# Kernel optimization log

Hardware: AMD Instinct MI355X
Metric: run time of the kernel (lower is better)

Reference implementation:

```python
import jax, jax.numpy as jnp
import numpy as np

N = 100000      # nodes
E = 1600000     # edges (avg degree 16)
IN = 256        # in_channels
HID = 128       # hidden_channels
K = 10          # APPNP propagation steps
ALPHA = 0.1     # APPNP teleport probability


def setup_inputs() -> dict:
    key = jax.random.key(0)
    k1, k2, k3 = jax.random.split(key, 3)
    features = jax.random.normal(k1, (N, IN), dtype=jnp.float32)
    W = jax.random.normal(k2, (IN, HID), dtype=jnp.float32) * (1.0 / np.sqrt(IN))
    b = jnp.zeros((HID,), dtype=jnp.float32)
    edge_index = jax.random.randint(k3, (2, E), 0, N, dtype=jnp.int32)
    return {"features": features, "W": W, "b": b, "edge_index": edge_index}


def _edge_norm(src, dst, n):
    # DGL GraphConv norm='both': D_out^{-1/2} at src, D_in^{-1/2} at dst
    ones = jnp.ones(src.shape, dtype=jnp.float32)
    deg_out = jax.ops.segment_sum(ones, src, num_segments=n)
    deg_in = jax.ops.segment_sum(ones, dst, num_segments=n)
    inv_out = jnp.where(deg_out > 0, jax.lax.rsqrt(jnp.maximum(deg_out, 1.0)), 0.0)
    inv_in = jnp.where(deg_in > 0, jax.lax.rsqrt(jnp.maximum(deg_in, 1.0)), 0.0)
    return inv_out[src] * inv_in[dst]  # [E] per-edge coefficient


def _propagate(h, src, dst, enorm, n):
    # gather src features, scale by symmetric norm, scatter-add to dst
    m = h[src] * enorm[:, None]                       # [E, HID]
    return jax.ops.segment_sum(m, dst, num_segments=n)


def reference(features, W, b, edge_index):
    n = features.shape[0]
    src, dst = edge_index[0], edge_index[1]
    enorm = _edge_norm(src, dst, n)

    # GraphConv: project then aggregate (feat dropout is identity in eval)
    h = features @ W                                  # [N, HID]
    h = _propagate(h, src, dst, enorm, n) + b
    h = jax.nn.relu(h)

    # APPNP: h_{t+1} = (1-alpha) * A_hat h_t + alpha * h_0 (edge_drop off in eval)
    h0 = h

    def step(hc, _):
        hn = (1.0 - ALPHA) * _propagate(hc, src, dst, enorm, n) + ALPHA * h0
        return hn, None

    h, _ = jax.lax.scan(step, h, None, length=K)
    return h
```

## Files before the change

kernel.cpp:

```cpp
#include <hip/hip_runtime.h>
#include <hip/hip_fp16.h>
#include <stdint.h>

#define N_NODES 100000
#define N_EDGES 1600000
#define IN_CH 256
#define HID 128
#define K_STEPS 10
#define ALPHA 0.1f

#define BKT_BITS 9
#define BKT_SIZE 512
#define NBKT 196
#define HBLK 256
#define EPB (N_EDGES / HBLK)

#define DR 8
#define DRS (N_NODES / DR)
#define DC 32
#define DCE (N_EDGES / DC)

static __global__ __launch_bounds__(256) void bucket_hist_kernel(const int* __restrict__ dst,
                                                                 uint32_t* __restrict__ partials) {
    __shared__ uint32_t h[NBKT];
    int b = blockIdx.x, t = threadIdx.x;
    if (t < NBKT) h[t] = 0;
    __syncthreads();
    int base = b * EPB;
    for (int i = t; i < EPB; i += 256)
        atomicAdd(&h[(unsigned)dst[base + i] >> BKT_BITS], 1u);
    __syncthreads();
    if (t < NBKT) partials[t * HBLK + b] = h[t];
}

static __global__ __launch_bounds__(256) void srcdeg_hist_kernel(const int* __restrict__ src,
                                                                 uint16_t* __restrict__ srcpart) {
    __shared__ uint32_t h[DRS];
    int r = blockIdx.x >> 5;
    int c = blockIdx.x & 31;
    int t = threadIdx.x;
    for (int i = t; i < DRS; i += 256) h[i] = 0;
    __syncthreads();
    int lo = r * DRS;
    int base = c * DCE;
    for (int i = t; i < DCE; i += 256) {
        unsigned sl = (unsigned)(src[base + i] - lo);
        if (sl < DRS) atomicAdd(&h[sl], 1u);
    }
    __syncthreads();
    for (int i = t; i < DRS; i += 256)
        srcpart[(size_t)c * N_NODES + lo + i] = (uint16_t)h[i];
}

static __global__ void srcdeg_reduce_kernel(const uint16_t* __restrict__ srcpart,
                                            float* __restrict__ inv_out) {
    int n = blockIdx.x * 256 + threadIdx.x;
    if (n >= N_NODES) return;
    uint32_t d = 0;
#pragma unroll
    for (int c = 0; c < DC; c++) d += srcpart[(size_t)c * N_NODES + n];
    inv_out[n] = d ? rsqrtf((float)d) : 0.f;
}

static __global__ __launch_bounds__(64) void bucket_totals_kernel(const uint32_t* __restrict__ partials,
                                                                  uint32_t* __restrict__ totals) {
    int k = blockIdx.x, t = threadIdx.x;
    const uint32_t* row = partials + (size_t)k * HBLK;
    uint32_t s = row[t] + row[t + 64] + row[t + 128] + row[t + 192];
#pragma unroll
    for (int o = 32; o; o >>= 1) s += __shfl_down(s, o);
    if (t == 0) totals[k] = s;
}

static __global__ __launch_bounds__(256) void bucket_cursor_kernel(const uint32_t* __restrict__ partials,
                                                                   const uint32_t* __restrict__ totals,
                                                                   uint32_t* __restrict__ blockCursor,
                                                                   uint32_t* __restrict__ bucket_base) {
    __shared__ uint32_t sc[256];
    int k = blockIdx.x, t = threadIdx.x;
    uint32_t tk = (t < NBKT) ? totals[t] : 0;
    sc[t] = tk;
    __syncthreads();
    for (int o = 1; o < 256; o <<= 1) {
        uint32_t u = (t >= o) ? sc[t - o] : 0;
        __syncthreads();
        sc[t] += u;
        __syncthreads();
    }
    uint32_t incl_k = sc[k];
    uint32_t total_k = totals[k];
    uint32_t base = incl_k - total_k;
    if (t == 0) {
        bucket_base[k] = base;
        if (k == NBKT - 1) bucket_base[NBKT] = incl_k;
    }
    __syncthreads();
    uint32_t p = partials[(size_t)k * HBLK + t];
    sc[t] = p;
    __syncthreads();
    for (int o = 1; o < 256; o <<= 1) {
        uint32_t u = (t >= o) ? sc[t - o] : 0;
        __syncthreads();
        sc[t] += u;
        __syncthreads();
    }
    blockCursor[(size_t)k * HBLK + t] = base + sc[t] - p;
}

static __global__ __launch_bounds__(256) void bucket_scatter_kernel(const int* __restrict__ src,
                                                                    const int* __restrict__ dst,
                                                                    const uint32_t* __restrict__ blockCursor,
                                                                    int2* __restrict__ ebuf) {
    __shared__ uint32_t cur[NBKT];
    int b = blockIdx.x, t = threadIdx.x;
    if (t < NBKT) cur[t] = blockCursor[(size_t)t * HBLK + b];
    __syncthreads();
    int base = b * EPB;
    for (int i = t; i < EPB; i += 256) {
        int s = src[base + i], d = dst[base + i];
        uint32_t p = atomicAdd(&cur[(unsigned)d >> BKT_BITS], 1u);
        ebuf[p] = make_int2(s, d);
    }
}

static __global__ __launch_bounds__(256) void bucket_build_kernel(const int2* __restrict__ ebuf,
                                                                  const uint32_t* __restrict__ bucket_base,
                                                                  int* __restrict__ row_ptr,
                                                                  float* __restrict__ inv_in,
                                                                  int* __restrict__ csr) {
    __shared__ uint32_t h[BKT_SIZE];
    __shared__ uint32_t rs[BKT_SIZE];
    __shared__ uint32_t ps[256];
    int k = blockIdx.x, t = threadIdx.x;
    uint32_t b0 = bucket_base[k], b1 = bucket_base[k + 1];
    h[t] = 0; h[t + 256] = 0;
    __syncthreads();
    for (uint32_t i = b0 + t; i < b1; i += 256)
        atomicAdd(&h[ebuf[i].y & (BKT_SIZE - 1)], 1u);
    __syncthreads();
    uint32_t a = h[2 * t], bb = h[2 * t + 1];
    uint32_t pair = a + bb;
    ps[t] = pair;
    __syncthreads();
    for (int o = 1; o < 256; o <<= 1) {
        uint32_t u = (t >= o) ? ps[t - o] : 0;
        __syncthreads();
        ps[t] += u;
        __syncthreads();
    }
    uint32_t ex = ps[t] - pair;
    rs[2 * t] = ex;
    rs[2 * t + 1] = ex + a;
    int node0 = k * BKT_SIZE;
    if (node0 + 2 * t < N_NODES) {
        row_ptr[node0 + 2 * t] = (int)(b0 + ex);
        inv_in[node0 + 2 * t] = a ? rsqrtf((float)a) : 0.f;
    }
    if (node0 + 2 * t + 1 < N_NODES) {
        row_ptr[node0 + 2 * t + 1] = (int)(b0 + ex + a);
        inv_in[node0 + 2 * t + 1] = bb ? rsqrtf((float)bb) : 0.f;
    }
    if (k == NBKT - 1 && t == 0) row_ptr[N_NODES] = (int)b1;
    __syncthreads();
    for (uint32_t i = b0 + t; i < b1; i += 256) {
        int2 e = ebuf[i];
        int li = e.y & (BKT_SIZE - 1);
        uint32_t p = atomicAdd(&rs[li], 1u);
        csr[b0 + p] = e.x;
    }
}

static __global__ __launch_bounds__(256) void gemm_kernel(const float* __restrict__ A,
                                                          const float* __restrict__ B,
                                                          const float* __restrict__ inv_out,
                                                          __half* __restrict__ t16) {
    __shared__ float As[32][68];
    __shared__ float Bs[32][128];
    int tid = threadIdx.x;
    int brow = blockIdx.x * 64;
    int tc = tid & 31, tr = tid >> 5;
    float acc[8][4] = {};
    for (int k0 = 0; k0 < IN_CH; k0 += 32) {
#pragma unroll
        for (int i = 0; i < 2; i++) {
            int l = (tid + i * 256) * 4;
            int r = l >> 5;
            int kk = l & 31;
            float4 a = make_float4(0.f, 0.f, 0.f, 0.f);
            int grow = brow + r;
            if (grow < N_NODES) a = *(const float4*)&A[(size_t)grow * IN_CH + k0 + kk];
            As[kk + 0][r] = a.x;
            As[kk + 1][r] = a.y;
            As[kk + 2][r] = a.z;
            As[kk + 3][r] = a.w;
        }
#pragma unroll
        for (int i = 0; i < 4; i++) {
            int l = (tid + i * 256) * 4;
            int kk = l >> 7;
            int cc = l & 127;
            *(float4*)&Bs[kk][cc] = *(const float4*)&B[(size_t)(k0 + kk) * HID + cc];
        }
        __syncthreads();
#pragma unroll
        for (int kk = 0; kk < 32; kk++) {
            float4 b4 = *(const float4*)&Bs[kk][tc * 4];
            float4 a0 = *(const float4*)&As[kk][tr * 8];
            float4 a1 = *(const float4*)&As[kk][tr * 8 + 4];
            float av[8] = {a0.x, a0.y, a0.z, a0.w, a1.x, a1.y, a1.z, a1.w};
#pragma unroll
            for (int i = 0; i < 8; i++) {
                acc[i][0] += av[i] * b4.x;
                acc[i][1] += av[i] * b4.y;
                acc[i][2] += av[i] * b4.z;
                acc[i][3] += av[i] * b4.w;
            }
        }
        __syncthreads();
    }
#pragma unroll
    for (int i = 0; i < 8; i++) {
        int grow = brow + tr * 8 + i;
        if (grow < N_NODES) {
            float sc = inv_out[grow];
            __half2 h01 = __floats2half2_rn(acc[i][0] * sc, acc[i][1] * sc);
            __half2 h23 = __floats2half2_rn(acc[i][2] * sc, acc[i][3] * sc);
            uint2 u;
            u.x = *(uint32_t*)&h01;
            u.y = *(uint32_t*)&h23;
            *(uint2*)&t16[(size_t)grow * HID + tc * 4] = u;
        }
    }
}

static __global__ void zero_rows_kernel(__half* a, __half* b, __half* c) {
    int t = threadIdx.x;
    ((uint32_t*)a)[(size_t)N_NODES * 64 + t] = 0;
    ((uint32_t*)b)[(size_t)N_NODES * 64 + t] = 0;
    ((uint32_t*)c)[(size_t)N_NODES * 64 + t] = 0;
}

template <int MODE>
static __global__ __launch_bounds__(256) void prop16_kernel(const __half* __restrict__ gin,
                                                            const int* __restrict__ rp,
                                                            const int* __restrict__ cs,
                                                            const float* __restrict__ inv_in,
                                                            const float* __restrict__ inv_out,
                                                            const float* __restrict__ bias,
                                                            const __half* __restrict__ h0h,
                                                            __half* __restrict__ gout,
                                                            __half* __restrict__ h0out,
                                                            float* __restrict__ fout) {
    int wid = (int)((blockIdx.x * 256u + threadIdx.x) >> 6);
    if (wid >= N_NODES) return;
    int lane = threadIdx.x & 63;
    int sub = lane >> 4;
    int cl = lane & 15;
    int s = rp[wid], e = rp[wid + 1];
    const uint4* g4 = (const uint4*)gin;

    float a[8] = {};
    for (int j = s; j < e; j += 8) {
        int j0 = j + sub, j1 = j0 + 4;
        int v0 = cs[j0], v1 = cs[j1];
        int i0 = (j0 < e) ? v0 : N_NODES;
        int i1 = (j1 < e) ? v1 : N_NODES;
        uint4 u0 = g4[(size_t)i0 * 16 + cl];
        uint4 u1 = g4[(size_t)i1 * 16 + cl];
        const __half2* p0 = (const __half2*)&u0;
        const __half2* p1 = (const __half2*)&u1;
#pragma unroll
        for (int k = 0; k < 4; k++) {
            float2 f0 = __half22float2(p0[k]);
            float2 f1 = __half22float2(p1[k]);
            a[2 * k] += f0.x + f1.x;
            a[2 * k + 1] += f0.y + f1.y;
        }
    }
#pragma unroll
    for (int k = 0; k < 8; k++) {
        a[k] += __shfl_xor(a[k], 16);
        a[k] += __shfl_xor(a[k], 32);
    }
    if (sub != 0) return;
    int c0 = cl * 8;
    if (MODE == 0) {
        float ii = inv_in[wid], io = inv_out[wid];
        float4 b0 = *(const float4*)&bias[c0];
        float4 b1 = *(const float4*)&bias[c0 + 4];
        float h[8];
        h[0] = fmaxf(a[0] * ii + b0.x, 0.f);
        h[1] = fmaxf(a[1] * ii + b0.y, 0.f);
        h[2] = fmaxf(a[2] * ii + b0.z, 0.f);
        h[3] = fmaxf(a[3] * ii + b0.w, 0.f);
        h[4] = fmaxf(a[4] * ii + b1.x, 0.f);
        h[5] = fmaxf(a[5] * ii + b1.y, 0.f);
        h[6] = fmaxf(a[6] * ii + b1.z, 0.f);
        h[7] = fmaxf(a[7] * ii + b1.w, 0.f);
        __half2 hh[4], gg[4];
#pragma unroll
        for (int k = 0; k < 4; k++) {
            hh[k] = __floats2half2_rn(h[2 * k], h[2 * k + 1]);
            gg[k] = __floats2half2_rn(h[2 * k] * io, h[2 * k + 1] * io);
        }
        ((uint4*)h0out)[(size_t)wid * 16 + cl] = *(uint4*)hh;
        ((uint4*)gout)[(size_t)wid * 16 + cl] = *(uint4*)gg;
    } else {
        float ii = inv_in[wid] * (1.f - ALPHA);
        uint4 uh = ((const uint4*)h0h)[(size_t)wid * 16 + cl];
        const __half2* ph = (const __half2*)&uh;
        float h[8];
#pragma unroll
        for (int k = 0; k < 4; k++) {
            float2 f = __half22float2(ph[k]);
            h[2 * k] = a[2 * k] * ii + ALPHA * f.x;
            h[2 * k + 1] = a[2 * k + 1] * ii + ALPHA * f.y;
        }
        if (MODE == 1) {
            float io = inv_out[wid];
            __half2 gg[4];
#pragma unroll
            for (int k = 0; k < 4; k++)
                gg[k] = __floats2half2_rn(h[2 * k] * io, h[2 * k + 1] * io);
            ((uint4*)gout)[(size_t)wid * 16 + cl] = *(uint4*)gg;
        } else {
            *(float4*)&fout[(size_t)wid * HID + c0] = make_float4(h[0], h[1], h[2], h[3]);
            *(float4*)&fout[(size_t)wid * HID + c0 + 4] = make_float4(h[4], h[5], h[6], h[7]);
        }
    }
}

extern "C" void kernel_launch(void* const* d_in, const int* in_sizes, int n_in,
                              void* d_out, int out_size, void* d_ws, size_t ws_size,
                              hipStream_t stream) {
    const float* features = (const float*)d_in[0];
    const float* W = (const float*)d_in[1];
    const float* b = (const float*)d_in[2];
    const int* edge_index = (const int*)d_in[3];
    const int* src = edge_index;
    const int* dst = edge_index + N_EDGES;
    float* out = (float*)d_out;

    char* ws = (char*)d_ws;
    size_t off = 0;
    auto alloc = [&](size_t bytes) -> void* {
        void* p = ws + off;
        off = (off + bytes + 255) & ~(size_t)255;
        return p;
    };
    int* csr = (int*)alloc(((size_t)N_EDGES + 8) * 4);
    __half* t16 = (__half*)alloc((size_t)(N_NODES + 1) * HID * 2);
    __half* gA  = (__half*)alloc((size_t)(N_NODES + 1) * HID * 2);
    __half* gB  = (__half*)alloc((size_t)(N_NODES + 1) * HID * 2);
    __half* h0h = (__half*)alloc((size_t)N_NODES * HID * 2);
    float* inv_out = (float*)alloc((size_t)N_NODES * 4);
    float* inv_in = (float*)alloc((size_t)N_NODES * 4);
    int* row_ptr = (int*)alloc((size_t)(N_NODES + 1) * 4);
    char* tb = (char*)gA;
    size_t toff = 0;
    auto talloc = [&](size_t bytes) -> void* {
        void* p = tb + toff;
        toff = (toff + bytes + 255) & ~(size_t)255;
        return p;
    };
    int2* ebuf = (int2*)talloc((size_t)N_EDGES * 8);
    uint16_t* srcpart = (uint16_t*)talloc((size_t)DC * N_NODES * 2);
    uint32_t* partials = (uint32_t*)talloc((size_t)NBKT * HBLK * 4);
    uint32_t* blockCursor = (uint32_t*)talloc((size_t)NBKT * HBLK * 4);
    uint32_t* totals = (uint32_t*)talloc(NBKT * 4);
    uint32_t* bucket_base = (uint32_t*)talloc((NBKT + 1) * 4);

    bucket_hist_kernel<<<HBLK, 256, 0, stream>>>(dst, partials);
    srcdeg_hist_kernel<<<DR * DC, 256, 0, stream>>>(src, srcpart);
    srcdeg_reduce_kernel<<<(N_NODES + 255) / 256, 256, 0, stream>>>(srcpart, inv_out);
    bucket_totals_kernel<<<NBKT, 64, 0, stream>>>(partials, totals);
    bucket_cursor_kernel<<<NBKT, 256, 0, stream>>>(partials, totals, blockCursor, bucket_base);
    bucket_scatter_kernel<<<HBLK, 256, 0, stream>>>(src, dst, blockCursor, ebuf);
    bucket_build_kernel<<<NBKT, 256, 0, stream>>>(ebuf, bucket_base, row_ptr, inv_in, csr);

    gemm_kernel<<<(N_NODES + 63) / 64, 256, 0, stream>>>(features, W, inv_out, t16);
    zero_rows_kernel<<<1, 64, 0, stream>>>(t16, gA, gB);

    int pb = (int)(((size_t)N_NODES * 64) / 256);
    prop16_kernel<0><<<pb, 256, 0, stream>>>(t16, row_ptr, csr, inv_in, inv_out, b, nullptr,
                                             gA, h0h, nullptr);
    const __half* cur = gA;
    for (int t = 0; t < K_STEPS - 1; t++) {
        __half* nxt = (t & 1) ? gA : gB;
        prop16_kernel<1><<<pb, 256, 0, stream>>>(cur, row_ptr, csr, inv_in, inv_out, nullptr, h0h,
                                                 nxt, nullptr, nullptr);
        cur = nxt;
    }
    prop16_kernel<2><<<pb, 256, 0, stream>>>(cur, row_ptr, csr, inv_in, inv_out, nullptr, h0h,
                                             nullptr, nullptr, out);
}
```

Baseline: 896.4 us.

## Replace FP32 SIMT projection GEMM with FP16 MFMA matrix-core GEMM

Swaps the scalar FP32 tiled GEMM for an MFMA 16x16x32 f16 kernel with 128-row tiles, swizzled shared-memory layout and a staged coalesced output write. A small kernel pre-transposes W to f16. The aim is to cut the compute-bound projection cost on the features×W step. In exchange, inputs are rounded to fp16 before multiplication, which may change accuracy slightly.

```diff
diff --git a/kernel.cpp b/kernel.cpp
--- a/kernel.cpp
+++ b/kernel.cpp
@@ -19,6 +19,9 @@
 #define DRS (N_NODES / DR)
 #define DC 32
 #define DCE (N_EDGES / DC)
+
+typedef _Float16 f16x8 __attribute__((ext_vector_type(8)));
+typedef float f32x4 __attribute__((ext_vector_type(4)));
 
 static __global__ __launch_bounds__(256) void bucket_hist_kernel(const int* __restrict__ dst,
                                                                  uint32_t* __restrict__ partials) {
@@ -170,65 +173,107 @@
     }
 }
 
-static __global__ __launch_bounds__(256) void gemm_kernel(const float* __restrict__ A,
-                                                          const float* __restrict__ B,
-                                                          const float* __restrict__ inv_out,
-                                                          __half* __restrict__ t16) {
-    __shared__ float As[32][68];
-    __shared__ float Bs[32][128];
+static __global__ __launch_bounds__(256) void wtrans_kernel(const float* __restrict__ W,
+                                                            _Float16* __restrict__ Wt) {
+    int k = blockIdx.x * 2 + (threadIdx.x >> 7);
+    int c = threadIdx.x & 127;
+    Wt[(size_t)c * IN_CH + k] = (_Float16)W[(size_t)k * HID + c];
+}
+
+__device__ __forceinline__ int kswz(int row, int kb) {
+    return (kb ^ ((row ^ (row >> 2)) & 3)) << 3;
+}
+
+static __global__ __launch_bounds__(256) void mfma_gemm_kernel(const float* __restrict__ A,
+                                                               const _Float16* __restrict__ Wt,
+                                                               const float* __restrict__ inv_out,
+                                                               __half* __restrict__ t16) {
+    __shared__ _Float16 As[128][32];
+    __shared__ _Float16 Bs[128][32];
+    __shared__ __half  Cs[128][HID];
+    __shared__ float   io[128];
     int tid = threadIdx.x;
-    int brow = blockIdx.x * 64;
-    int tc = tid & 31, tr = tid >> 5;
-    float acc[8][4] = {};
+    int brow = blockIdx.x * 128;
+    if (tid < 128) {
+        int r = brow + tid;
+        io[tid] = (r < N_NODES) ? inv_out[r] : 0.f;
+    }
+    int wave = tid >> 6, lane = tid & 63;
+    int wm = wave >> 1, wn = wave & 1;
+    int l15 = lane & 15, l4 = lane >> 4;
+
+    f32x4 acc[4][4] = {};
+    int srow = tid >> 1;
+    int sko = (tid & 1) * 16;
+
     for (int k0 = 0; k0 < IN_CH; k0 += 32) {
-#pragma unroll
-        for (int i = 0; i < 2; i++) {
-            int l = (tid + i * 256) * 4;
-            int r = l >> 5;
-            int kk = l & 31;
-            float4 a = make_float4(0.f, 0.f, 0.f, 0.f);
-            int grow = brow + r;
-            if (grow < N_NODES) a = *(const float4*)&A[(size_t)grow * IN_CH + k0 + kk];
-            As[kk + 0][r] = a.x;
-            As[kk + 1][r] = a.y;
-            As[kk + 2][r] = a.z;
-            As[kk + 3][r] = a.w;
-        }
-#pragma unroll
-        for (int i = 0; i < 4; i++) {
-            int l = (tid + i * 256) * 4;
-            int kk = l >> 7;
-            int cc = l & 127;
-            *(float4*)&Bs[kk][cc] = *(const float4*)&B[(size_t)(k0 + kk) * HID + cc];
-        }
-        __syncthreads();
-#pragma unroll
-        for (int kk = 0; kk < 32; kk++) {
-            float4 b4 = *(const float4*)&Bs[kk][tc * 4];
-            float4 a0 = *(const float4*)&As[kk][tr * 8];
-            float4 a1 = *(const float4*)&As[kk][tr * 8 + 4];
-            float av[8] = {a0.x, a0.y, a0.z, a0.w, a1.x, a1.y, a1.z, a1.w};
-#pragma unroll
-            for (int i = 0; i < 8; i++) {
-                acc[i][0] += av[i] * b4.x;
-                acc[i][1] += av[i] * b4.y;
-                acc[i][2] += av[i] * b4.z;
-                acc[i][3] += av[i] * b4.w;
+        {
+            float4 f[4];
+            int gr = brow + srow;
+            if (gr < N_NODES) {
+                const float4* ap = (const float4*)&A[(size_t)gr * IN_CH + k0 + sko];
+                f[0] = ap[0]; f[1] = ap[1]; f[2] = ap[2]; f[3] = ap[3];
+            } else {
+                f[0] = f[1] = f[2] = f[3] = make_float4(0.f, 0.f, 0.f, 0.f);
             }
-        }
-        __syncthreads();
-    }
-#pragma unroll
-    for (int i = 0; i < 8; i++) {
-        int grow = brow + tr * 8 + i;
-        if (grow < N_NODES) {
-            float sc = inv_out[grow];
-            __half2 h01 = __floats2half2_rn(acc[i][0] * sc, acc[i][1] * sc);
-            __half2 h23 = __floats2half2_rn(acc[i][2] * sc, acc[i][3] * sc);
-            uint2 u;
-            u.x = *(uint32_t*)&h01;
-            u.y = *(uint32_t*)&h23;
-            *(uint2*)&t16[(size_t)grow * HID + tc * 4] = u;
+#pragma unroll
+            for (int g = 0; g < 2; g++) {
+                _Float16 hh[8];
+                float* fp = (float*)&f[2 * g];
+#pragma unroll
+                for (int q = 0; q < 8; q++) hh[q] = (_Float16)fp[q];
+                int kb = (sko >> 3) + g;
+                *(uint4*)&As[srow][kswz(srow, kb)] = *(uint4*)hh;
+            }
+        }
+        {
+            const uint4* wp = (const uint4*)&Wt[(size_t)srow * IN_CH + k0 + sko];
+            uint4 u0 = wp[0], u1 = wp[1];
+            int kb = sko >> 3;
+            *(uint4*)&Bs[srow][kswz(srow, kb)] = u0;
+            *(uint4*)&Bs[srow][kswz(srow, kb + 1)] = u1;
+        }
+        __syncthreads();
+        f16x8 af[4], bf[4];
+#pragma unroll
+        for (int mt = 0; mt < 4; mt++) {
+            int row = wm * 64 + mt * 16 + l15;
+            af[mt] = *(f16x8*)&As[row][kswz(row, l4)];
+        }
+#pragma unroll
+        for (int nt = 0; nt < 4; nt++) {
+            int col = wn * 64 + nt * 16 + l15;
+            bf[nt] = *(f16x8*)&Bs[col][kswz(col, l4)];
+        }
+#pragma unroll
+        for (int mt = 0; mt < 4; mt++)
+#pragma unroll
+            for (int nt = 0; nt < 4; nt++)
+                acc[mt][nt] = __builtin_amdgcn_mfma_f32_16x16x32_f16(af[mt], bf[nt], acc[mt][nt], 0, 0, 0);
+        __syncthreads();
+    }
+#pragma unroll
+    for (int mt = 0; mt < 4; mt++) {
+#pragma unroll
+        for (int nt = 0; nt < 4; nt++) {
+#pragma unroll
+            for (int r = 0; r < 4; r++) {
+                int row = wm * 64 + mt * 16 + l4 * 4 + r;
+                int col = wn * 64 + nt * 16 + l15;
+                Cs[row][col] = __float2half(acc[mt][nt][r] * io[row]);
+            }
+        }
+    }
+    __syncthreads();
+    {
+        int row = tid >> 1;
+        int c0 = (tid & 1) * 64;
+        int gr = brow + row;
+        if (gr < N_NODES) {
+            uint4* s = (uint4*)&Cs[row][c0];
+            uint4* d = (uint4*)&t16[(size_t)gr * HID + c0];
+#pragma unroll
+            for (int i = 0; i < 8; i++) d[i] = s[i];
         }
     }
 }
@@ -356,6 +401,7 @@
     float* inv_out = (float*)alloc((size_t)N_NODES * 4);
     float* inv_in = (float*)alloc((size_t)N_NODES * 4);
     int* row_ptr = (int*)alloc((size_t)(N_NODES + 1) * 4);
+    _Float16* Wt = (_Float16*)alloc((size_t)HID * IN_CH * 2);
     char* tb = (char*)gA;
     size_t toff = 0;
     auto talloc = [&](size_t bytes) -> void* {
@@ -378,7 +424,8 @@
     bucket_scatter_kernel<<<HBLK, 256, 0, stream>>>(src, dst, blockCursor, ebuf);
     bucket_build_kernel<<<NBKT, 256, 0, stream>>>(ebuf, bucket_base, row_ptr, inv_in, csr);
 
-    gemm_kernel<<<(N_NODES + 63) / 64, 256, 0, stream>>>(features, W, inv_out, t16);
+    wtrans_kernel<<<128, 256, 0, stream>>>(W, Wt);
+    mfma_gemm_kernel<<<(N_NODES + 127) / 128, 256, 0, stream>>>(features, Wt, inv_out, t16);
     zero_rows_kernel<<<1, 64, 0, stream>>>(t16, gA, gB);
 
     int pb = (int)(((size_t)N_NODES * 64) / 256);
```

New measurement: 838.4 us. -6.5%, faster.
